# Performance work log

Hardware: AMD Instinct MI355X
Metric: run time of the kernel (lower is better)

Reference implementation:

```python
import jax, jax.numpy as jnp
import numpy as np

N = 50000      # nodes per graph
E = 600000     # edges per graph
IN_DIM = 512
HID = 128
LAYERS = 2


def setup_inputs() -> dict:
    key = jax.random.key(0)
    ks = jax.random.split(key, 24)
    s = 0.05
    inp = {
        "src_fea": jax.random.normal(ks[0], (N, IN_DIM), jnp.float32),
        "trg_fea": jax.random.normal(ks[1], (N, IN_DIM), jnp.float32),
        "src_row": jax.random.randint(ks[2], (E,), 0, N, jnp.int32),
        "src_col": jax.random.randint(ks[3], (E,), 0, N, jnp.int32),
        "trg_row": jax.random.randint(ks[4], (E,), 0, N, jnp.int32),
        "trg_col": jax.random.randint(ks[5], (E,), 0, N, jnp.int32),
        # fx: Linear(in,hid)+GELU+Linear(hid,hid)+GELU
        "fxW1": jax.random.normal(ks[6], (IN_DIM, HID), jnp.float32) * s,
        "fxb1": jnp.zeros((HID,), jnp.float32),
        "fxW2": jax.random.normal(ks[7], (HID, HID), jnp.float32) * s,
        "fxb2": jnp.zeros((HID,), jnp.float32),
        # edge_att_mlp: Linear(2h,20)+ReLU+Linear(20,10)+ReLU+Linear(10,1)+ReLU
        "eaW1": jax.random.normal(ks[8], (2 * HID, 20), jnp.float32) * s,
        "eab1": jnp.zeros((20,), jnp.float32),
        "eaW2": jax.random.normal(ks[9], (20, 10), jnp.float32) * s,
        "eab2": jnp.zeros((10,), jnp.float32),
        "eaW3": jax.random.normal(ks[10], (10, 1), jnp.float32) * s,
        "eab3": jnp.zeros((1,), jnp.float32),
        # GraphConv (PyG-style, bias=False): out = x@Wroot + agg@Wrel
        "convWroot": jax.random.normal(ks[11], (LAYERS, HID, HID), jnp.float32) * s,
        "convWrel": jax.random.normal(ks[12], (LAYERS, HID, HID), jnp.float32) * s,
    }
    return inp


def _fx(x, W1, b1, W2, b2):
    h = jax.nn.gelu(x @ W1 + b1, approximate=False)
    return jax.nn.gelu(h @ W2 + b2, approximate=False)


def _edge_att(e, eaW1, eab1, eaW2, eab2, eaW3, eab3):
    h = jax.nn.relu(e @ eaW1 + eab1)
    h = jax.nn.relu(h @ eaW2 + eab2)
    h = jax.nn.relu(h @ eaW3 + eab3)
    return jax.nn.sigmoid(h)  # [E,1]


def _graph_conv(x, row, col, ew, Wroot, Wrel):
    # message from source (row) gathered, weighted, aggregated at target (col)
    msg = ew[:, None] * x[row]                                  # [E,h]
    agg = jax.ops.segment_sum(msg, col, num_segments=N)         # [N,h]
    return x @ Wroot + agg @ Wrel


def _branch(x0, row, col, convWroot, convWrel, eaW1, eab1, eaW2, eab2, eaW3, eab3, hard):
    xs, cfds = [], []
    x = x0
    for i in range(LAYERS):
        edge_rep = jnp.concatenate([x[row], x[col]], axis=-1)    # [E,2h]
        att = _edge_att(edge_rep, eaW1, eab1, eaW2, eab2, eaW3, eab3)[:, 0]
        wc = (att + hard) * 0.5
        wo = 1.0 - wc
        x = jax.nn.soft_sign(_graph_conv(x, row, col, wc, convWroot[i], convWrel[i]))
        cfd = jax.nn.soft_sign(_graph_conv(x, row, col, wo, convWroot[i], convWrel[i]))
        xs.append(x)
        cfds.append(cfd)
    return xs, cfds


def reference(src_fea, trg_fea, src_row, src_col, trg_row, trg_col,
              fxW1, fxb1, fxW2, fxb2,
              eaW1, eab1, eaW2, eab2, eaW3, eab3,
              convWroot, convWrel):
    src1 = _fx(src_fea, fxW1, fxb1, fxW2, fxb2)
    trg1 = _fx(trg_fea, fxW1, fxb1, fxW2, fxb2)
    ea = (eaW1, eab1, eaW2, eab2, eaW3, eab3)
    xs_s, cf_s = _branch(src1, src_row, src_col, convWroot, convWrel, *ea, 0.0)
    xs_t, cf_t = _branch(trg1, trg_row, trg_col, convWroot, convWrel, *ea, 0.0)
    # stack: [src1, xs_s..., trg1, xs_t..., cf_s..., cf_t...] -> [2+2*LAYERS+2*LAYERS? no: 10, N, h]
    return jnp.stack([src1] + xs_s + [trg1] + xs_t + cf_s + cf_t, axis=0)
```

## Files before the change

kernel.cpp:

```cpp
#include <hip/hip_runtime.h>
#include <math.h>
#include <stdint.h>


typedef __attribute__((ext_vector_type(8))) short bh8;
typedef __attribute__((ext_vector_type(4))) float f4;

__device__ __forceinline__ float relu_f(float x) { return x > 0.f ? x : 0.f; }

__device__ __forceinline__ unsigned short f2bf(float f) {
    union { float f; unsigned u; } v; v.f = f;
    unsigned r = v.u + 0x7FFF + ((v.u >> 16) & 1);
    return (unsigned short)(r >> 16);
}
__device__ __forceinline__ float bf2f(unsigned short b) {
    union { unsigned u; float f; } v; v.u = ((unsigned)b) << 16;
    return v.f;
}

template<int ACT>
__device__ __forceinline__ float act_fn(float x) {
    if (ACT == 1) return 0.5f * x * (1.f + erff(x * 0.70710678118654752f));
    if (ACT == 2) return x / (1.f + fabsf(x));
    return x;
}

__device__ __forceinline__ float edge_att_mlp(const unsigned short* p1,
                                              const unsigned short* p2,
                                              const float* w2, const float* b2s,
                                              const float* w3s, const float* sb1,
                                              float sb3)
{
    bh8 a0 = *(const bh8*)&p1[0];
    bh8 a1 = *(const bh8*)&p1[8];
    ushort4 a2 = *(const ushort4*)&p1[16];
    bh8 b0 = *(const bh8*)&p2[0];
    bh8 b1 = *(const bh8*)&p2[8];
    ushort4 b2 = *(const ushort4*)&p2[16];

    float h1[20];
    #pragma unroll
    for (int j = 0; j < 8; ++j)
        h1[j] = relu_f(bf2f((unsigned short)a0[j]) + bf2f((unsigned short)b0[j]) + sb1[j]);
    #pragma unroll
    for (int j = 0; j < 8; ++j)
        h1[8 + j] = relu_f(bf2f((unsigned short)a1[j]) + bf2f((unsigned short)b1[j]) + sb1[8 + j]);
    h1[16] = relu_f(bf2f(a2.x) + bf2f(b2.x) + sb1[16]);
    h1[17] = relu_f(bf2f(a2.y) + bf2f(b2.y) + sb1[17]);
    h1[18] = relu_f(bf2f(a2.z) + bf2f(b2.z) + sb1[18]);
    h1[19] = relu_f(bf2f(a2.w) + bf2f(b2.w) + sb1[19]);

    float h3 = sb3;
    #pragma unroll
    for (int j2 = 0; j2 < 10; ++j2) {
        float s = b2s[j2];
        #pragma unroll
        for (int j = 0; j < 20; ++j)
            s = fmaf(h1[j], w2[j * 10 + j2], s);
        h3 = fmaf(relu_f(s), w3s[j2], h3);
    }
    h3 = relu_f(h3);
    return 1.f / (1.f + expf(-h3));
}

__device__ __forceinline__ void emit_p_phase(short* As, short* Bs,
                                             const short* __restrict__ W56,
                                             short* __restrict__ P,
                                             int row0, int M, int t)
{
    #pragma unroll
    for (int p = 0; p < 4; ++p) {
        int idx = t + 256 * p;
        int r = idx >> 4;
        int c = (idx & 15) * 8;
        *(bh8*)&Bs[r * 136 + c] = *(const bh8*)(W56 + r * 128 + c);
    }
    __syncthreads();
    const int lane = t & 63, w = t >> 6, l15 = lane & 15, l4 = lane >> 4;
    f4 accP[4];
    #pragma unroll
    for (int ni = 0; ni < 4; ++ni) accP[ni] = (f4){0.f, 0.f, 0.f, 0.f};
    #pragma unroll
    for (int kk = 0; kk < 4; ++kk) {
        bh8 a = *(const bh8*)&As[(w * 16 + l15) * 136 + kk * 32 + l4 * 8];
        #pragma unroll
        for (int ni = 0; ni < 4; ++ni) {
            bh8 b = *(const bh8*)&Bs[(ni * 16 + l15) * 136 + kk * 32 + l4 * 8];
            accP[ni] = __builtin_amdgcn_mfma_f32_16x16x32_bf16(a, b, accP[ni], 0, 0, 0);
        }
    }
    #pragma unroll
    for (int ni = 0; ni < 4; ++ni) {
        int col = ni * 16 + l15;
        #pragma unroll
        for (int r = 0; r < 4; ++r) {
            int row = row0 + w * 16 + l4 * 4 + r;
            if (row < M) P[(size_t)row * 64 + col] = (short)f2bf(accP[ni][r]);
        }
    }
}

template<int K, int AF, int ACT, bool BIAS, bool WF32, bool WB16, bool EMITP>
__global__ __launch_bounds__(256, 2)
void mfma_gemm(const void* __restrict__ X0a, const void* __restrict__ X0b,
               const short* __restrict__ W0t, const float* __restrict__ bias,
               float* __restrict__ outfA, short* __restrict__ outbA,
               float* __restrict__ outfB, short* __restrict__ outbB,
               const short* __restrict__ W56,
               short* __restrict__ PA, short* __restrict__ PB, int M)
{
    constexpr int BK  = 64;
    constexpr int LDA = EMITP ? 136 : 72;
    __shared__ short As[64 * LDA];
    __shared__ short Bs[128 * 72];

    const int half = gridDim.x >> 1;
    int bid = blockIdx.x;
    const int g1 = bid >= half;
    bid -= g1 ? half : 0;
    const void* X0v = g1 ? X0b : X0a;
    float* outf = g1 ? outfB : outfA;
    short* outb = g1 ? outbB : outbA;
    short* P    = g1 ? PB : PA;

    const int t    = threadIdx.x;
    const int row0 = bid * 64;
    const int lane = t & 63;
    const int w    = t >> 6;
    const int wr   = w & 1;
    const int wc   = w >> 1;
    const int l15  = lane & 15;
    const int l4   = lane >> 4;

    f4 acc[2][4];
    #pragma unroll
    for (int i = 0; i < 2; ++i)
        #pragma unroll
        for (int j = 0; j < 4; ++j)
            acc[i][j] = (f4){0.f, 0.f, 0.f, 0.f};

    const int ar = t >> 3;
    const int ac = (t & 7) * 8;

    #pragma unroll 1
    for (int k0 = 0; k0 < K; k0 += BK) {
        __syncthreads();
        #pragma unroll
        for (int p = 0; p < 2; ++p) {
            int r    = ar + p * 32;
            int grow = row0 + r;
            bh8 sv = {0, 0, 0, 0, 0, 0, 0, 0};
            if (AF == 0) {
                if (grow < M) {
                    const float* src = (const float*)X0v + (size_t)grow * K + k0 + ac;
                    float4 v0 = *(const float4*)src;
                    float4 v1 = *(const float4*)(src + 4);
                    sv[0] = (short)f2bf(v0.x); sv[1] = (short)f2bf(v0.y);
                    sv[2] = (short)f2bf(v0.z); sv[3] = (short)f2bf(v0.w);
                    sv[4] = (short)f2bf(v1.x); sv[5] = (short)f2bf(v1.y);
                    sv[6] = (short)f2bf(v1.z); sv[7] = (short)f2bf(v1.w);
                }
            } else {
                if (grow < M)
                    sv = *(const bh8*)((const short*)X0v + (size_t)grow * K + k0 + ac);
            }
            *(bh8*)&As[r * LDA + ac] = sv;
        }
        #pragma unroll
        for (int p = 0; p < 4; ++p) {
            int r = ar + p * 32;
            *(bh8*)&Bs[r * 72 + ac] = *(const bh8*)(W0t + (size_t)r * K + k0 + ac);
        }
        __syncthreads();
        #pragma unroll
        for (int kk = 0; kk < 2; ++kk) {
            bh8 a[2], b[4];
            #pragma unroll
            for (int mi = 0; mi < 2; ++mi)
                a[mi] = *(const bh8*)&As[(wr*32 + mi*16 + l15) * LDA + kk*32 + l4*8];
            #pragma unroll
            for (int ni = 0; ni < 4; ++ni)
                b[ni] = *(const bh8*)&Bs[(wc*64 + ni*16 + l15) * 72 + kk*32 + l4*8];
            #pragma unroll
            for (int mi = 0; mi < 2; ++mi)
                #pragma unroll
                for (int ni = 0; ni < 4; ++ni)
                    acc[mi][ni] = __builtin_amdgcn_mfma_f32_16x16x32_bf16(
                        a[mi], b[ni], acc[mi][ni], 0, 0, 0);
        }
    }

    if (EMITP) __syncthreads();
    #pragma unroll
    for (int mi = 0; mi < 2; ++mi) {
        #pragma unroll
        for (int ni = 0; ni < 4; ++ni) {
            int col = wc * 64 + ni * 16 + l15;
            float bv = BIAS ? bias[col] : 0.f;
            #pragma unroll
            for (int r = 0; r < 4; ++r) {
                int rloc = wr * 32 + mi * 16 + l4 * 4 + r;
                int row  = row0 + rloc;
                float v = act_fn<ACT>(acc[mi][ni][r] + bv);
                unsigned short bb = f2bf(v);
                if (row < M) {
                    if (WF32) outf[(size_t)row * 128 + col] = v;
                    if (WB16) outb[(size_t)row * 128 + col] = (short)bb;
                }
                if (EMITP) As[rloc * LDA + col] = (short)bb;
            }
        }
    }
    if (EMITP) emit_p_phase(As, Bs, W56, P, row0, M, t);
}

template<int MODE, bool WB16, bool EMITP>
__global__ __launch_bounds__(256, 2)
void conv_fused(const short* __restrict__ XbA, const short* __restrict__ XbB,
                const int* __restrict__ coffA, const int* __restrict__ coffB,
                const int* __restrict__ crowA, const int* __restrict__ crowB,
                const float* __restrict__ attcA, const float* __restrict__ attcB,
                const short* __restrict__ Wroot, const short* __restrict__ Wrel,
                const short* __restrict__ W56,
                float* __restrict__ outfA, float* __restrict__ outfB,
                short* __restrict__ outbA, short* __restrict__ outbB,
                short* __restrict__ PA, short* __restrict__ PB, int M)
{
    constexpr int LDA = 136;
    __shared__ short As[64 * LDA];
    __shared__ short Bs[128 * 72];

    const int half = gridDim.x >> 1;
    int bid = blockIdx.x;
    const int g1 = bid >= half;
    bid -= g1 ? half : 0;
    const short* Xb   = g1 ? XbB   : XbA;
    const int*   coff = g1 ? coffB : coffA;
    const int*   crow = g1 ? crowB : crowA;
    const float* attc = g1 ? attcB : attcA;
    float* outf = g1 ? outfB : outfA;
    short* outb = g1 ? outbB : outbA;
    short* P    = g1 ? PB : PA;

    const int t    = threadIdx.x;
    const int row0 = bid * 64;
    const int lane = t & 63;
    const int w    = t >> 6;
    const int wr   = w & 1;
    const int wc   = w >> 1;
    const int l15  = lane & 15;
    const int l4   = lane >> 4;

    {
        const int g  = t >> 4;
        const int li = t & 15;
        #pragma unroll 1
        for (int q = 0; q < 4; ++q) {
            int rloc = g * 4 + q;
            int n = row0 + rloc;
            float a8[8] = {0.f, 0.f, 0.f, 0.f, 0.f, 0.f, 0.f, 0.f};
            if (n < M) {
                int p  = coff[n];
                int pe = coff[n + 1];
                for (; p + 7 < pe; p += 8) {
                    float w0 = attc[p],     w1 = attc[p + 1];
                    float w2 = attc[p + 2], w3 = attc[p + 3];
                    float w4 = attc[p + 4], w5 = attc[p + 5];
                    float w6 = attc[p + 6], w7 = attc[p + 7];
                    int r0 = crow[p],     r1 = crow[p + 1];
                    int r2 = crow[p + 2], r3 = crow[p + 3];
                    int r4 = crow[p + 4], r5 = crow[p + 5];
                    int r6 = crow[p + 6], r7 = crow[p + 7];
                    w0 = MODE ? fmaf(-0.5f, w0, 1.f) : 0.5f * w0;
                    w1 = MODE ? fmaf(-0.5f, w1, 1.f) : 0.5f * w1;
                    w2 = MODE ? fmaf(-0.5f, w2, 1.f) : 0.5f * w2;
                    w3 = MODE ? fmaf(-0.5f, w3, 1.f) : 0.5f * w3;
                    w4 = MODE ? fmaf(-0.5f, w4, 1.f) : 0.5f * w4;
                    w5 = MODE ? fmaf(-0.5f, w5, 1.f) : 0.5f * w5;
                    w6 = MODE ? fmaf(-0.5f, w6, 1.f) : 0.5f * w6;
                    w7 = MODE ? fmaf(-0.5f, w7, 1.f) : 0.5f * w7;
                    bh8 v0 = *(const bh8*)&Xb[(size_t)r0 * 128 + li * 8];
                    bh8 v1 = *(const bh8*)&Xb[(size_t)r1 * 128 + li * 8];
                    bh8 v2 = *(const bh8*)&Xb[(size_t)r2 * 128 + li * 8];
                    bh8 v3 = *(const bh8*)&Xb[(size_t)r3 * 128 + li * 8];
                    bh8 v4 = *(const bh8*)&Xb[(size_t)r4 * 128 + li * 8];
                    bh8 v5 = *(const bh8*)&Xb[(size_t)r5 * 128 + li * 8];
                    bh8 v6 = *(const bh8*)&Xb[(size_t)r6 * 128 + li * 8];
                    bh8 v7 = *(const bh8*)&Xb[(size_t)r7 * 128 + li * 8];
                    #pragma unroll
                    for (int j = 0; j < 8; ++j) {
                        a8[j] = fmaf(w0, bf2f((unsigned short)v0[j]), a8[j]);
                        a8[j] = fmaf(w1, bf2f((unsigned short)v1[j]), a8[j]);
                        a8[j] = fmaf(w2, bf2f((unsigned short)v2[j]), a8[j]);
                        a8[j] = fmaf(w3, bf2f((unsigned short)v3[j]), a8[j]);
                        a8[j] = fmaf(w4, bf2f((unsigned short)v4[j]), a8[j]);
                        a8[j] = fmaf(w5, bf2f((unsigned short)v5[j]), a8[j]);
                        a8[j] = fmaf(w6, bf2f((unsigned short)v6[j]), a8[j]);
                        a8[j] = fmaf(w7, bf2f((unsigned short)v7[j]), a8[j]);
                    }
                }
                for (; p + 3 < pe; p += 4) {
                    float w0 = attc[p],     w1 = attc[p + 1];
                    float w2 = attc[p + 2], w3 = attc[p + 3];
                    int r0 = crow[p],     r1 = crow[p + 1];
                    int r2 = crow[p + 2], r3 = crow[p + 3];
                    w0 = MODE ? fmaf(-0.5f, w0, 1.f) : 0.5f * w0;
                    w1 = MODE ? fmaf(-0.5f, w1, 1.f) : 0.5f * w1;
                    w2 = MODE ? fmaf(-0.5f, w2, 1.f) : 0.5f * w2;
                    w3 = MODE ? fmaf(-0.5f, w3, 1.f) : 0.5f * w3;
                    bh8 v0 = *(const bh8*)&Xb[(size_t)r0 * 128 + li * 8];
                    bh8 v1 = *(const bh8*)&Xb[(size_t)r1 * 128 + li * 8];
                    bh8 v2 = *(const bh8*)&Xb[(size_t)r2 * 128 + li * 8];
                    bh8 v3 = *(const bh8*)&Xb[(size_t)r3 * 128 + li * 8];
                    #pragma unroll
                    for (int j = 0; j < 8; ++j) {
                        a8[j] = fmaf(w0, bf2f((unsigned short)v0[j]), a8[j]);
                        a8[j] = fmaf(w1, bf2f((unsigned short)v1[j]), a8[j]);
                        a8[j] = fmaf(w2, bf2f((unsigned short)v2[j]), a8[j]);
                        a8[j] = fmaf(w3, bf2f((unsigned short)v3[j]), a8[j]);
                    }
                }
                for (; p < pe; ++p) {
                    float w0 = attc[p];
                    int   r0 = crow[p];
                    w0 = MODE ? fmaf(-0.5f, w0, 1.f) : 0.5f * w0;
                    bh8 v0 = *(const bh8*)&Xb[(size_t)r0 * 128 + li * 8];
                    #pragma unroll
                    for (int j = 0; j < 8; ++j)
                        a8[j] = fmaf(w0, bf2f((unsigned short)v0[j]), a8[j]);
                }
            }
            bh8 o;
            #pragma unroll
            for (int j = 0; j < 8; ++j) o[j] = (short)f2bf(a8[j]);
            *(bh8*)&As[rloc * LDA + li * 8] = o;
        }
    }
    __syncthreads();

    f4 acc[2][4];
    #pragma unroll
    for (int i = 0; i < 2; ++i)
        #pragma unroll
        for (int j = 0; j < 4; ++j)
            acc[i][j] = (f4){0.f, 0.f, 0.f, 0.f};

    const int ar = t >> 3;
    const int ac = (t & 7) * 8;

    #pragma unroll 1
    for (int k0 = 0; k0 < 128; k0 += 64) {
        if (k0) __syncthreads();
        #pragma unroll
        for (int p = 0; p < 4; ++p) {
            int r = ar + p * 32;
            *(bh8*)&Bs[r * 72 + ac] = *(const bh8*)(Wrel + (size_t)r * 128 + k0 + ac);
        }
        __syncthreads();
        #pragma unroll
        for (int kk = 0; kk < 2; ++kk) {
            bh8 a[2], b[4];
            #pragma unroll
            for (int mi = 0; mi < 2; ++mi)
                a[mi] = *(const bh8*)&As[(wr*32 + mi*16 + l15) * LDA + k0 + kk*32 + l4*8];
            #pragma unroll
            for (int ni = 0; ni < 4; ++ni)
                b[ni] = *(const bh8*)&Bs[(wc*64 + ni*16 + l15) * 72 + kk*32 + l4*8];
            #pragma unroll
            for (int mi = 0; mi < 2; ++mi)
                #pragma unroll
                for (int ni = 0; ni < 4; ++ni)
                    acc[mi][ni] = __builtin_amdgcn_mfma_f32_16x16x32_bf16(
                        a[mi], b[ni], acc[mi][ni], 0, 0, 0);
        }
    }

    #pragma unroll 1
    for (int k0 = 0; k0 < 128; k0 += 64) {
        __syncthreads();
        #pragma unroll
        for (int p = 0; p < 2; ++p) {
            int r    = ar + p * 32;
            int grow = row0 + r;
            bh8 sv = {0, 0, 0, 0, 0, 0, 0, 0};
            if (grow < M)
                sv = *(const bh8*)(Xb + (size_t)grow * 128 + k0 + ac);
            *(bh8*)&As[r * LDA + ac] = sv;
        }
        #pragma unroll
        for (int p = 0; p < 4; ++p) {
            int r = ar + p * 32;
            *(bh8*)&Bs[r * 72 + ac] = *(const bh8*)(Wroot + (size_t)r * 128 + k0 + ac);
        }
        __syncthreads();
        #pragma unroll
        for (int kk = 0; kk < 2; ++kk) {
            bh8 a[2], b[4];
            #pragma unroll
            for (int mi = 0; mi < 2; ++mi)
                a[mi] = *(const bh8*)&As[(wr*32 + mi*16 + l15) * LDA + kk*32 + l4*8];
            #pragma unroll
            for (int ni = 0; ni < 4; ++ni)
                b[ni] = *(const bh8*)&Bs[(wc*64 + ni*16 + l15) * 72 + kk*32 + l4*8];
            #pragma unroll
            for (int mi = 0; mi < 2; ++mi)
                #pragma unroll
                for (int ni = 0; ni < 4; ++ni)
                    acc[mi][ni] = __builtin_amdgcn_mfma_f32_16x16x32_bf16(
                        a[mi], b[ni], acc[mi][ni], 0, 0, 0);
        }
    }

    if (EMITP) __syncthreads();
    #pragma unroll
    for (int mi = 0; mi < 2; ++mi) {
        #pragma unroll
        for (int ni = 0; ni < 4; ++ni) {
            int col = wc * 64 + ni * 16 + l15;
            #pragma unroll
            for (int r = 0; r < 4; ++r) {
                int rloc = wr * 32 + mi * 16 + l4 * 4 + r;
                int row  = row0 + rloc;
                float v = act_fn<2>(acc[mi][ni][r]);
                unsigned short bb = f2bf(v);
                if (row < M) {
                    outf[(size_t)row * 128 + col] = v;
                    if (WB16) outb[(size_t)row * 128 + col] = (short)bb;
                }
                if (EMITP) As[rloc * LDA + col] = (short)bb;
            }
        }
    }
    if (EMITP) emit_p_phase(As, Bs, W56, P, row0, M, t);
}

__global__ void prep_hist(const float* __restrict__ eaW1, const float* __restrict__ fxW1,
                          const float* __restrict__ fxW2, const float* __restrict__ convWroot,
                          const float* __restrict__ convWrel,
                          short* __restrict__ w56, short* __restrict__ fxW1t,
                          short* __restrict__ fxW2t, short* __restrict__ wrt,
                          short* __restrict__ wlt,
                          const int* __restrict__ colS, const int* __restrict__ colT,
                          int* __restrict__ deg, int N, int E, int prepBlocks)
{
    if ((int)blockIdx.x >= prepBlocks) {
        int idx = (blockIdx.x - prepBlocks) * 256 + threadIdx.x;
        if (idx >= 2 * E) return;
        const int g1 = idx >= E;
        const int e  = idx - (g1 ? E : 0);
        int c = (g1 ? colT : colS)[e];
        atomicAdd(&deg[(size_t)g1 * N + c], 1);
        return;
    }
    int i = blockIdx.x * 256 + threadIdx.x;
    if (i < 64 * 128) {
        int j = i >> 7, k = i & 127;
        float v = 0.f;
        if (j < 20)                  v = eaW1[k * 20 + j];
        else if (j >= 32 && j < 52)  v = eaW1[(128 + k) * 20 + (j - 32)];
        w56[i] = (short)f2bf(v);
        return;
    }
    i -= 64 * 128;
    if (i < 512 * 128) {
        int k = i >> 7, n = i & 127;
        fxW1t[(size_t)n * 512 + k] = (short)f2bf(fxW1[i]);
        return;
    }
    i -= 512 * 128;
    if (i < 128 * 128) {
        int k = i >> 7, n = i & 127;
        fxW2t[n * 128 + k] = (short)f2bf(fxW2[i]);
        return;
    }
    i -= 128 * 128;
    if (i < 2 * 128 * 128) {
        int L = i >> 14, r = i & 16383;
        int k = r >> 7, n = r & 127;
        wrt[L * 16384 + n * 128 + k] = (short)f2bf(convWroot[i]);
        return;
    }
    i -= 2 * 128 * 128;
    if (i < 2 * 128 * 128) {
        int L = i >> 14, r = i & 16383;
        int k = r >> 7, n = r & 127;
        wlt[L * 16384 + n * 128 + k] = (short)f2bf(convWrel[i]);
    }
}

__global__ __launch_bounds__(256)
void edge_att_both(const short* __restrict__ PS, const short* __restrict__ PT,
                   const int* __restrict__ rowS, const int* __restrict__ colS,
                   const int* __restrict__ rowT, const int* __restrict__ colT,
                   const int* __restrict__ eposS, const int* __restrict__ eposT,
                   const float* __restrict__ eab1, const float* __restrict__ eaW2,
                   const float* __restrict__ eab2, const float* __restrict__ eaW3,
                   const float* __restrict__ eab3,
                   float* __restrict__ attcS, float* __restrict__ attcT, int E)
{
    __shared__ float w2[200], b2s[10], w3s[10], sb1[20], sb3;
    int t = threadIdx.x;
    if (t < 200) w2[t] = eaW2[t];
    if (t < 20)  sb1[t] = eab1[t];
    if (t < 10)  { b2s[t] = eab2[t]; w3s[t] = eaW3[t]; }
    if (t == 0)  sb3 = eab3[0];
    __syncthreads();

    int idx = blockIdx.x * 256 + t;
    if (idx >= 2 * E) return;
    const int g1 = idx >= E;
    const int e  = idx - (g1 ? E : 0);
    const short* P    = g1 ? PT : PS;
    const int*   row  = g1 ? rowT : rowS;
    const int*   col  = g1 ? colT : colS;
    const int*   epos = g1 ? eposT : eposS;
    float*       attc = g1 ? attcT : attcS;

    int r = row[e], c = col[e];
    const unsigned short* p1 = (const unsigned short*)P + (size_t)r * 64;
    const unsigned short* p2 = (const unsigned short*)P + (size_t)c * 64 + 32;
    attc[epos[e]] = edge_att_mlp(p1, p2, w2, b2s, w3s, sb1, sb3);
}

__device__ __forceinline__ int block_incl_scan(int v, int* wsum)
{
    int lane = threadIdx.x & 63;
    int w    = threadIdx.x >> 6;
    #pragma unroll
    for (int off = 1; off < 64; off <<= 1) {
        int t = __shfl_up(v, off);
        if (lane >= off) v += t;
    }
    if (lane == 63) wsum[w] = v;
    __syncthreads();
    int add = 0;
    for (int j = 0; j < w; ++j) add += wsum[j];
    return v + add;
}

__global__ __launch_bounds__(256)
void scanA_both(const int* __restrict__ deg, int* __restrict__ coffS,
                int* __restrict__ coffT, int* __restrict__ bsum, int N)
{
    __shared__ int wsum[4];
    int gy = blockIdx.y;
    const int* d = deg + (size_t)gy * N;
    int* coff    = gy ? coffT : coffS;
    int* bs      = bsum + gy * 256;
    int i = blockIdx.x * 256 + threadIdx.x;
    int orig = (i < N) ? d[i] : 0;
    int v = block_incl_scan(orig, wsum);
    if (i < N) coff[i] = v - orig;
    if (threadIdx.x == 255) bs[blockIdx.x] = v;
}

__global__ __launch_bounds__(256)
void scanB_both(const int* __restrict__ bsum, int* __restrict__ boff, int nb)
{
    __shared__ int wsum[4];
    int gy = blockIdx.y;
    const int* bs = bsum + gy * 256;
    int* bo       = boff + gy * 256;
    int tid = threadIdx.x;
    int orig = (tid < nb) ? bs[tid] : 0;
    int v = block_incl_scan(orig, wsum);
    if (tid < nb) bo[tid] = v - orig;
}

__global__ __launch_bounds__(256)
void scanC_both(int* __restrict__ coffS, int* __restrict__ coffT,
                const int* __restrict__ boff, int* __restrict__ curS,
                int* __restrict__ curT, int N, int E)
{
    int gy = blockIdx.y;
    int* coff = gy ? coffT : coffS;
    int* cur  = gy ? curT  : curS;
    const int* bo = boff + gy * 256;
    int i = blockIdx.x * 256 + threadIdx.x;
    if (i < N) {
        int v = coff[i] + bo[i >> 8];
        coff[i] = v;
        cur[i]  = v;
    }
    if (i == 0) coff[N] = E;
}

__global__ __launch_bounds__(256)
void fill_att_both(const int* __restrict__ rowS, const int* __restrict__ colS,
                   const int* __restrict__ rowT, const int* __restrict__ colT,
                   int* __restrict__ curS, int* __restrict__ curT,
                   int* __restrict__ crowS, int* __restrict__ crowT,
                   int* __restrict__ eposS, int* __restrict__ eposT,
                   const short* __restrict__ PS, const short* __restrict__ PT,
                   const float* __restrict__ eab1, const float* __restrict__ eaW2,
                   const float* __restrict__ eab2, const float* __restrict__ eaW3,
                   const float* __restrict__ eab3,
                   float* __restrict__ attcS, float* __restrict__ attcT, int E)
{
    __shared__ float w2[200], b2s[10], w3s[10], sb1[20], sb3;
    int t = threadIdx.x;
    if (t < 200) w2[t] = eaW2[t];
    if (t < 20)  sb1[t] = eab1[t];
    if (t < 10)  { b2s[t] = eab2[t]; w3s[t] = eaW3[t]; }
    if (t == 0)  sb3 = eab3[0];
    __syncthreads();

    int idx = blockIdx.x * 256 + t;
    if (idx >= 2 * E) return;
    const int g1 = idx >= E;
    const int e  = idx - (g1 ? E : 0);
    const int* row = g1 ? rowT : rowS;
    const int* col = g1 ? colT : colS;
    int* cur  = g1 ? curT  : curS;
    int* crow = g1 ? crowT : crowS;
    int* epos = g1 ? eposT : eposS;
    const short* P = g1 ? PT : PS;
    float* attc    = g1 ? attcT : attcS;

    int c = col[e];
    int r = row[e];
    int p = atomicAdd(&cur[c], 1);
    crow[p] = r;
    epos[e] = p;

    const unsigned short* p1 = (const unsigned short*)P + (size_t)r * 64;
    const unsigned short* p2 = (const unsigned short*)P + (size_t)c * 64 + 32;
    attc[p] = edge_att_mlp(p1, p2, w2, b2s, w3s, sb1, sb3);
}


extern "C" void kernel_launch(void* const* d_in, const int* in_sizes, int n_in,
                              void* d_out, int out_size, void* d_ws, size_t ws_size,
                              hipStream_t stream)
{
    const float* src_fea = (const float*)d_in[0];
    const float* trg_fea = (const float*)d_in[1];
    const int*   src_row = (const int*)d_in[2];
    const int*   src_col = (const int*)d_in[3];
    const int*   trg_row = (const int*)d_in[4];
    const int*   trg_col = (const int*)d_in[5];
    const float* fxW1 = (const float*)d_in[6];
    const float* fxb1 = (const float*)d_in[7];
    const float* fxW2 = (const float*)d_in[8];
    const float* fxb2 = (const float*)d_in[9];
    const float* eaW1 = (const float*)d_in[10];
    const float* eab1 = (const float*)d_in[11];
    const float* eaW2 = (const float*)d_in[12];
    const float* eab2 = (const float*)d_in[13];
    const float* eaW3 = (const float*)d_in[14];
    const float* eab3 = (const float*)d_in[15];
    const float* convWroot = (const float*)d_in[16];
    const float* convWrel  = (const float*)d_in[17];

    const int N = in_sizes[0] / 512;
    const int E = in_sizes[2];

    float* out = (float*)d_out;
    const size_t slot_sz = (size_t)N * 128;
    auto slot = [&](int i) { return out + (size_t)i * slot_sz; };

    float* fp    = (float*)d_ws;
    float* attcS = fp; fp += E;
    float* attcT = fp; fp += E;
    int* ip    = (int*)fp;
    int* deg   = ip; ip += 2 * N;
    int* bsum  = ip; ip += 512;
    int* boff  = ip; ip += 512;
    int* coffS = ip; ip += N + 2;
    int* coffT = ip; ip += N + 2;
    int* curS  = ip; ip += N;
    int* curT  = ip; ip += N;
    int* crowS = ip; ip += E;
    int* crowT = ip; ip += E;
    int* eposS = ip; ip += E;
    int* eposT = ip; ip += E;
    short* sp = (short*)((((uintptr_t)ip) + 255) & ~(uintptr_t)255);
    short* xb0   = sp; sp += slot_sz;
    short* xb1   = sp; sp += slot_sz;
    short* xsbS[2]; short* xsbT[2];
    xsbS[0] = sp; sp += slot_sz;
    xsbS[1] = sp; sp += slot_sz;
    xsbT[0] = sp; sp += slot_sz;
    xsbT[1] = sp; sp += slot_sz;
    short* PS    = sp; sp += (size_t)N * 64;
    short* PT    = sp; sp += (size_t)N * 64;
    short* w56   = sp; sp += 64 * 128;
    short* fxW1t = sp; sp += 128 * 512;
    short* fxW2t = sp; sp += 128 * 128;
    short* wrt   = sp; sp += 2 * 128 * 128;
    short* wlt   = sp; sp += 2 * 128 * 128;

    const int e2grid  = (2 * E + 255) / 256;
    const int nchunks = (N + 255) / 256;

    hipMemsetAsync(deg, 0, (size_t)2 * N * sizeof(int), stream);
    const int prep_total = 64*128 + 512*128 + 128*128 + 2*128*128 + 2*128*128;
    const int prepBlocks = (prep_total + 255) / 256;
    prep_hist<<<prepBlocks + e2grid, 256, 0, stream>>>(
        eaW1, fxW1, fxW2, convWroot, convWrel, w56, fxW1t, fxW2t, wrt, wlt,
        src_col, trg_col, deg, N, E, prepBlocks);

    const int gb = (N + 63) / 64;
    short* hS = xsbS[0];
    short* hT = xsbT[0];
    mfma_gemm<512, 0, 1, true, false, true, false><<<2 * gb, 256, 0, stream>>>(
        src_fea, trg_fea, fxW1t, fxb1,
        nullptr, hS, nullptr, hT, nullptr, nullptr, nullptr, N);
    mfma_gemm<128, 1, 1, true, true, true, true><<<2 * gb, 256, 0, stream>>>(
        hS, hT, fxW2t, fxb2,
        slot(0), xb0, slot(3), xb1, w56, PS, PT, N);

    scanA_both<<<dim3(nchunks, 2), 256, 0, stream>>>(deg, coffS, coffT, bsum, N);
    scanB_both<<<dim3(1, 2), 256, 0, stream>>>(bsum, boff, nchunks);
    scanC_both<<<dim3(nchunks, 2), 256, 0, stream>>>(coffS, coffT, boff, curS, curT, N, E);
    fill_att_both<<<e2grid, 256, 0, stream>>>(
        src_row, src_col, trg_row, trg_col, curS, curT, crowS, crowT,
        eposS, eposT, PS, PT, eab1, eaW2, eab2, eaW3, eab3, attcS, attcT, E);

    short* xbS = xb0;
    short* xbT = xb1;
    for (int L = 0; L < 2; ++L) {
        float* xs_s = slot(1 + L);
        float* xs_t = slot(4 + L);
        float* cf_s = slot(6 + L);
        float* cf_t = slot(8 + L);
        const short* WrT = wrt + (size_t)L * 16384;
        const short* WlT = wlt + (size_t)L * 16384;

        if (L == 1)
            edge_att_both<<<e2grid, 256, 0, stream>>>(PS, PT, src_row, src_col,
                trg_row, trg_col, eposS, eposT, eab1, eaW2, eab2, eaW3, eab3,
                attcS, attcT, E);

        if (L == 0)
            conv_fused<0, true, true><<<2 * gb, 256, 0, stream>>>(
                xbS, xbT, coffS, coffT, crowS, crowT, attcS, attcT,
                WrT, WlT, w56, xs_s, xs_t, xsbS[L], xsbT[L], PS, PT, N);
        else
            conv_fused<0, true, false><<<2 * gb, 256, 0, stream>>>(
                xbS, xbT, coffS, coffT, crowS, crowT, attcS, attcT,
                WrT, WlT, nullptr, xs_s, xs_t, xsbS[L], xsbT[L], nullptr, nullptr, N);

        conv_fused<1, false, false><<<2 * gb, 256, 0, stream>>>(
            xsbS[L], xsbT[L], coffS, coffT, crowS, crowT, attcS, attcT,
            WrT, WlT, nullptr, cf_s, cf_t, nullptr, nullptr, nullptr, nullptr, N);

        xbS = xsbS[L];
        xbT = xsbT[L];
    }
}
```

Before: 594.3 us.

## Merge layer-1 edge attention into layer-0 counterfactual conv launch

The separate layer-1 edge-attention kernel is removed. Its work now runs as extra blocks appended to the grid of the layer-0 counterfactual conv kernel, writing into a second pair of attention buffers so the conv blocks can still read the layer-0 attention. This saves one kernel launch and lets the gather-heavy attention blocks share the GPU with the conv blocks. In exchange it costs double-buffered attention workspace, a larger grid in which two kinds of work compete for resources, and more kernel parameters.

```diff
diff --git a/kernel.cpp b/kernel.cpp
--- a/kernel.cpp
+++ b/kernel.cpp
@@ -214,7 +214,7 @@
     if (EMITP) emit_p_phase(As, Bs, W56, P, row0, M, t);
 }
 
-template<int MODE, bool WB16, bool EMITP>
+template<int MODE, bool WB16, bool EMITP, bool DOATT>
 __global__ __launch_bounds__(256, 2)
 void conv_fused(const short* __restrict__ XbA, const short* __restrict__ XbB,
                 const int* __restrict__ coffA, const int* __restrict__ coffB,
@@ -224,13 +224,50 @@
                 const short* __restrict__ W56,
                 float* __restrict__ outfA, float* __restrict__ outfB,
                 short* __restrict__ outbA, short* __restrict__ outbB,
-                short* __restrict__ PA, short* __restrict__ PB, int M)
+                short* __restrict__ PA, short* __restrict__ PB,
+                int convBlocks,
+                const int* __restrict__ rowS, const int* __restrict__ colS,
+                const int* __restrict__ rowT, const int* __restrict__ colT,
+                const int* __restrict__ eposS, const int* __restrict__ eposT,
+                const short* __restrict__ PinS, const short* __restrict__ PinT,
+                const float* __restrict__ eab1, const float* __restrict__ eaW2,
+                const float* __restrict__ eab2, const float* __restrict__ eaW3,
+                const float* __restrict__ eab3,
+                float* __restrict__ attOutS, float* __restrict__ attOutT,
+                int E, int M)
 {
     constexpr int LDA = 136;
     __shared__ short As[64 * LDA];
     __shared__ short Bs[128 * 72];
 
-    const int half = gridDim.x >> 1;
+    const int t = threadIdx.x;
+
+    if (DOATT && (int)blockIdx.x >= convBlocks) {
+        float* ea = (float*)As;
+        if (t < 200)       ea[t] = eaW2[t];
+        else if (t < 210)  ea[t] = eab2[t - 200];
+        else if (t < 220)  ea[t] = eaW3[t - 210];
+        else if (t < 240)  ea[t] = eab1[t - 220];
+        else if (t == 240) ea[240] = eab3[0];
+        __syncthreads();
+        int idx = ((int)blockIdx.x - convBlocks) * 256 + t;
+        if (idx < 2 * E) {
+            const int g1 = idx >= E;
+            const int e  = idx - (g1 ? E : 0);
+            const int* row  = g1 ? rowT  : rowS;
+            const int* col  = g1 ? colT  : colS;
+            const int* epos = g1 ? eposT : eposS;
+            const short* P  = g1 ? PinT  : PinS;
+            float* attOut   = g1 ? attOutT : attOutS;
+            int r = row[e], c = col[e];
+            const unsigned short* p1 = (const unsigned short*)P + (size_t)r * 64;
+            const unsigned short* p2 = (const unsigned short*)P + (size_t)c * 64 + 32;
+            attOut[epos[e]] = edge_att_mlp(p1, p2, ea, ea + 200, ea + 210, ea + 220, ea[240]);
+        }
+        return;
+    }
+
+    const int half = convBlocks >> 1;
     int bid = blockIdx.x;
     const int g1 = bid >= half;
     bid -= g1 ? half : 0;
@@ -242,7 +279,6 @@
     short* outb = g1 ? outbB : outbA;
     short* P    = g1 ? PB : PA;
 
-    const int t    = threadIdx.x;
     const int row0 = bid * 64;
     const int lane = t & 63;
     const int w    = t >> 6;
@@ -488,40 +524,6 @@
     }
 }
 
-__global__ __launch_bounds__(256)
-void edge_att_both(const short* __restrict__ PS, const short* __restrict__ PT,
-                   const int* __restrict__ rowS, const int* __restrict__ colS,
-                   const int* __restrict__ rowT, const int* __restrict__ colT,
-                   const int* __restrict__ eposS, const int* __restrict__ eposT,
-                   const float* __restrict__ eab1, const float* __restrict__ eaW2,
-                   const float* __restrict__ eab2, const float* __restrict__ eaW3,
-                   const float* __restrict__ eab3,
-                   float* __restrict__ attcS, float* __restrict__ attcT, int E)
-{
-    __shared__ float w2[200], b2s[10], w3s[10], sb1[20], sb3;
-    int t = threadIdx.x;
-    if (t < 200) w2[t] = eaW2[t];
-    if (t < 20)  sb1[t] = eab1[t];
-    if (t < 10)  { b2s[t] = eab2[t]; w3s[t] = eaW3[t]; }
-    if (t == 0)  sb3 = eab3[0];
-    __syncthreads();
-
-    int idx = blockIdx.x * 256 + t;
-    if (idx >= 2 * E) return;
-    const int g1 = idx >= E;
-    const int e  = idx - (g1 ? E : 0);
-    const short* P    = g1 ? PT : PS;
-    const int*   row  = g1 ? rowT : rowS;
-    const int*   col  = g1 ? colT : colS;
-    const int*   epos = g1 ? eposT : eposS;
-    float*       attc = g1 ? attcT : attcS;
-
-    int r = row[e], c = col[e];
-    const unsigned short* p1 = (const unsigned short*)P + (size_t)r * 64;
-    const unsigned short* p2 = (const unsigned short*)P + (size_t)c * 64 + 32;
-    attc[epos[e]] = edge_att_mlp(p1, p2, w2, b2s, w3s, sb1, sb3);
-}
-
 __device__ __forceinline__ int block_incl_scan(int v, int* wsum)
 {
     int lane = threadIdx.x & 63;
@@ -659,9 +661,11 @@
     const size_t slot_sz = (size_t)N * 128;
     auto slot = [&](int i) { return out + (size_t)i * slot_sz; };
 
-    float* fp    = (float*)d_ws;
-    float* attcS = fp; fp += E;
-    float* attcT = fp; fp += E;
+    float* fp     = (float*)d_ws;
+    float* attcS0 = fp; fp += E;
+    float* attcT0 = fp; fp += E;
+    float* attcS1 = fp; fp += E;
+    float* attcT1 = fp; fp += E;
     int* ip    = (int*)fp;
     int* deg   = ip; ip += 2 * N;
     int* bsum  = ip; ip += 512;
@@ -715,37 +719,37 @@
     scanC_both<<<dim3(nchunks, 2), 256, 0, stream>>>(coffS, coffT, boff, curS, curT, N, E);
     fill_att_both<<<e2grid, 256, 0, stream>>>(
         src_row, src_col, trg_row, trg_col, curS, curT, crowS, crowT,
-        eposS, eposT, PS, PT, eab1, eaW2, eab2, eaW3, eab3, attcS, attcT, E);
-
-    short* xbS = xb0;
-    short* xbT = xb1;
-    for (int L = 0; L < 2; ++L) {
-        float* xs_s = slot(1 + L);
-        float* xs_t = slot(4 + L);
-        float* cf_s = slot(6 + L);
-        float* cf_t = slot(8 + L);
-        const short* WrT = wrt + (size_t)L * 16384;
-        const short* WlT = wlt + (size_t)L * 16384;
-
-        if (L == 1)
-            edge_att_both<<<e2grid, 256, 0, stream>>>(PS, PT, src_row, src_col,
-                trg_row, trg_col, eposS, eposT, eab1, eaW2, eab2, eaW3, eab3,
-                attcS, attcT, E);
-
-        if (L == 0)
-            conv_fused<0, true, true><<<2 * gb, 256, 0, stream>>>(
-                xbS, xbT, coffS, coffT, crowS, crowT, attcS, attcT,
-                WrT, WlT, w56, xs_s, xs_t, xsbS[L], xsbT[L], PS, PT, N);
-        else
-            conv_fused<0, true, false><<<2 * gb, 256, 0, stream>>>(
-                xbS, xbT, coffS, coffT, crowS, crowT, attcS, attcT,
-                WrT, WlT, nullptr, xs_s, xs_t, xsbS[L], xsbT[L], nullptr, nullptr, N);
-
-        conv_fused<1, false, false><<<2 * gb, 256, 0, stream>>>(
-            xsbS[L], xsbT[L], coffS, coffT, crowS, crowT, attcS, attcT,
-            WrT, WlT, nullptr, cf_s, cf_t, nullptr, nullptr, nullptr, nullptr, N);
-
-        xbS = xsbS[L];
-        xbT = xsbT[L];
-    }
-}
+        eposS, eposT, PS, PT, eab1, eaW2, eab2, eaW3, eab3, attcS0, attcT0, E);
+
+    const short* WrT0 = wrt;
+    const short* WlT0 = wlt;
+    const short* WrT1 = wrt + 16384;
+    const short* WlT1 = wlt + 16384;
+
+    conv_fused<0, true, true, false><<<2 * gb, 256, 0, stream>>>(
+        xb0, xb1, coffS, coffT, crowS, crowT, attcS0, attcT0,
+        WrT0, WlT0, w56, slot(1), slot(4), xsbS[0], xsbT[0], PS, PT,
+        2 * gb, nullptr, nullptr, nullptr, nullptr, nullptr, nullptr,
+        nullptr, nullptr, nullptr, nullptr, nullptr, nullptr, nullptr,
+        nullptr, nullptr, E, N);
+
+    conv_fused<1, false, false, true><<<2 * gb + e2grid, 256, 0, stream>>>(
+        xsbS[0], xsbT[0], coffS, coffT, crowS, crowT, attcS0, attcT0,
+        WrT0, WlT0, nullptr, slot(6), slot(8), nullptr, nullptr, nullptr, nullptr,
+        2 * gb, src_row, src_col, trg_row, trg_col, eposS, eposT,
+        PS, PT, eab1, eaW2, eab2, eaW3, eab3, attcS1, attcT1, E, N);
+
+    conv_fused<0, true, false, false><<<2 * gb, 256, 0, stream>>>(
+        xsbS[0], xsbT[0], coffS, coffT, crowS, crowT, attcS1, attcT1,
+        WrT1, WlT1, nullptr, slot(2), slot(5), xsbS[1], xsbT[1], nullptr, nullptr,
+        2 * gb, nullptr, nullptr, nullptr, nullptr, nullptr, nullptr,
+        nullptr, nullptr, nullptr, nullptr, nullptr, nullptr, nullptr,
+        nullptr, nullptr, E, N);
+
+    conv_fused<1, false, false, false><<<2 * gb, 256, 0, stream>>>(
+        xsbS[1], xsbT[1], coffS, coffT, crowS, crowT, attcS1, attcT1,
+        WrT1, WlT1, nullptr, slot(7), slot(9), nullptr, nullptr, nullptr, nullptr,
+        2 * gb, nullptr, nullptr, nullptr, nullptr, nullptr, nullptr,
+        nullptr, nullptr, nullptr, nullptr, nullptr, nullptr, nullptr,
+        nullptr, nullptr, E, N);
+}
```

After: 590.2 us (median of 2 runs). Within noise of the previous version (-0.7%).
